# Performance work log

Hardware: AMD Instinct MI355X
Metric: run time of the kernel (lower is better)

## Reference

```python
import jax, jax.numpy as jnp
import numpy as np

N = 100000
DIN = 896        # 128 * 7, hard-coded as input_dim1 in hccexplorer_graph
HID = 256        # hidden_channels
HEADS = 1        # num_heads
L = 2            # num_layers
ALPHA = 0.5
EPS = 1e-5


def layernorm(x, g, b):
    m = jnp.mean(x, axis=-1, keepdims=True)
    v = jnp.mean((x - m) ** 2, axis=-1, keepdims=True)
    return (x - m) / jnp.sqrt(v + EPS) * g + b


def full_attention_conv(qs, ks, vs):
    # qs, ks, vs: [N, H, D]. NOTE: global Frobenius-norm normalization (no dim arg in torch.norm).
    n = qs.shape[0]
    qs = qs / jnp.linalg.norm(qs)
    ks = ks / jnp.linalg.norm(ks)
    kvs = jnp.einsum('lhm,lhd->hmd', ks, vs)                 # [H, D, D]
    attn_num = jnp.einsum('nhm,hmd->nhd', qs, kvs) + n * vs  # [N, H, D]
    ks_sum = jnp.sum(ks, axis=0)                             # [H, D]
    denom = jnp.einsum('nhm,hm->nh', qs, ks_sum)[..., None] + n
    return attn_num / denom                                  # [N, H, D]


def setup_inputs() -> dict:
    key = jax.random.key(0)
    ks = jax.random.split(key, 12)
    s_in = 1.0 / np.sqrt(DIN)
    s_h = 1.0 / np.sqrt(HID)
    inp = {
        'x': jax.random.normal(ks[0], (N, DIN), jnp.float32),
        'edge_index': jax.random.randint(ks[1], (2, 1600000), 0, N, jnp.int64),
        'fc_w': jax.random.uniform(ks[2], (DIN, HID), jnp.float32, -s_in, s_in),
        'fc_b': jax.random.uniform(ks[3], (HID,), jnp.float32, -s_in, s_in),
        'Wq': jax.random.uniform(ks[4], (L, HID, HEADS * HID), jnp.float32, -s_h, s_h),
        'Wk': jax.random.uniform(ks[5], (L, HID, HEADS * HID), jnp.float32, -s_h, s_h),
        'Wv': jax.random.uniform(ks[6], (L, HID, HEADS * HID), jnp.float32, -s_h, s_h),
        'bq': jax.random.uniform(ks[7], (L, HEADS * HID), jnp.float32, -s_h, s_h),
        'bk': jax.random.uniform(ks[8], (L, HEADS * HID), jnp.float32, -s_h, s_h),
        'bv': jax.random.uniform(ks[9], (L, HEADS * HID), jnp.float32, -s_h, s_h),
        'ln_g': 1.0 + 0.01 * jax.random.normal(ks[10], (L + 1, HID), jnp.float32),
        'ln_b': 0.01 * jax.random.normal(ks[11], (L + 1, HID), jnp.float32),
    }
    return inp


def reference(x, edge_index, fc_w, fc_b, Wq, Wk, Wv, bq, bk, bv, ln_g, ln_b):
    # TransConv.forward in eval mode (dropout disabled); edge_index unused by linear attention.
    h = x @ fc_w + fc_b
    h = layernorm(h, ln_g[0], ln_b[0])
    h = jax.nn.relu(h)
    prev = h
    for i in range(L):
        q = (h @ Wq[i] + bq[i]).reshape(-1, HEADS, HID)
        k = (h @ Wk[i] + bk[i]).reshape(-1, HEADS, HID)
        v = (h @ Wv[i] + bv[i]).reshape(-1, HEADS, HID)
        a = full_attention_conv(q, k, v).mean(axis=1)        # [N, HID]
        h = ALPHA * a + (1.0 - ALPHA) * prev                  # residual
        h = layernorm(h, ln_g[i + 1], ln_b[i + 1])
        prev = h
    return h
```

## Files before the change

### kernel.cpp

```cpp
#include <hip/hip_runtime.h>
#include <hip/hip_bf16.h>

#define GLOBAL_AS __attribute__((address_space(1)))
#define SHARED_AS __attribute__((address_space(3)))

typedef __attribute__((ext_vector_type(8))) __bf16 bf16x8;
typedef __attribute__((ext_vector_type(4))) float floatx4;

__device__ __forceinline__ void async_ld16(const void* g, void* l) {
    __builtin_amdgcn_global_load_lds((GLOBAL_AS void*)g, (SHARED_AS void*)l, 16, 0, 0);
}

__device__ __forceinline__ bf16x8 cvt8(float4 a, float4 b) {
    bf16x8 w;
    w[0] = (__bf16)a.x; w[1] = (__bf16)a.y; w[2] = (__bf16)a.z; w[3] = (__bf16)a.w;
    w[4] = (__bf16)b.x; w[5] = (__bf16)b.y; w[6] = (__bf16)b.z; w[7] = (__bf16)b.w;
    return w;
}

__global__ void __launch_bounds__(256) prep_kernel(
    const float* __restrict__ fc_w, const float* __restrict__ Wv,
    __bf16* __restrict__ fcwT, __bf16* __restrict__ WvT)
{
    int idx = blockIdx.x * 256 + threadIdx.x;
    if (idx < 256 * 896) {
        int n = idx / 896, k = idx - n * 896;
        fcwT[idx] = (__bf16)fc_w[k * 256 + n];
    } else {
        int j = idx - 256 * 896;
        int l = j >> 16;
        int r = j & 65535;
        int n = r >> 8, k = r & 255;
        WvT[j] = (__bf16)Wv[l * 65536 + k * 256 + n];
    }
}

template<int MODE>
__device__ __forceinline__ void ln_epilogue(
    floatx4 (&acc)[4][4], floatx4 (&hprev)[4][4],
    const float* __restrict__ bias, const float* __restrict__ g,
    const float* __restrict__ bb, __bf16* sH, void* scratch,
    float* __restrict__ Out, int m0, int M, int tid)
{
    const int wave = tid >> 6, lane = tid & 63;
    const int q = lane >> 4, c15 = lane & 15;
    const int wn = wave;

    float bj[4];
#pragma unroll
    for (int j = 0; j < 4; ++j) bj[j] = bias[wn * 64 + j * 16 + c15];
#pragma unroll
    for (int i = 0; i < 4; ++i)
#pragma unroll
        for (int j = 0; j < 4; ++j)
#pragma unroll
            for (int r = 0; r < 4; ++r) {
                float v = acc[i][j][r] + bj[j];
                if (MODE != 0) v = 0.5f * v + 0.5f * hprev[i][j][r];
                acc[i][j][r] = v;
            }

    float s[4][4], s2[4][4];
#pragma unroll
    for (int i = 0; i < 4; ++i)
#pragma unroll
        for (int r = 0; r < 4; ++r) {
            float t = 0.f, t2 = 0.f;
#pragma unroll
            for (int j = 0; j < 4; ++j) { float v = acc[i][j][r]; t += v; t2 += v * v; }
            s[i][r] = t; s2[i][r] = t2;
        }
#pragma unroll
    for (int m = 1; m < 16; m <<= 1)
#pragma unroll
        for (int i = 0; i < 4; ++i)
#pragma unroll
            for (int r = 0; r < 4; ++r) {
                s[i][r]  += __shfl_xor(s[i][r],  m);
                s2[i][r] += __shfl_xor(s2[i][r], m);
            }

    float2* part  = (float2*)scratch;
    float2* muinv = part + 256;
    if (c15 == 0) {
#pragma unroll
        for (int i = 0; i < 4; ++i)
#pragma unroll
            for (int r = 0; r < 4; ++r) {
                int rl = i * 16 + q * 4 + r;
                part[rl * 4 + wn] = make_float2(s[i][r], s2[i][r]);
            }
    }
    __syncthreads();
    if (tid < 64) {
        float S = 0.f, SS = 0.f;
#pragma unroll
        for (int w = 0; w < 4; ++w) { float2 p = part[tid * 4 + w]; S += p.x; SS += p.y; }
        float mu  = S * (1.f / 256.f);
        float var = SS * (1.f / 256.f) - mu * mu;
        muinv[tid] = make_float2(mu, rsqrtf(var + 1e-5f));
    }
    __syncthreads();

    float gj[4], bj2[4];
#pragma unroll
    for (int j = 0; j < 4; ++j) {
        int col = wn * 64 + j * 16 + c15;
        gj[j] = g[col]; bj2[j] = bb[col];
    }
#pragma unroll
    for (int i = 0; i < 4; ++i)
#pragma unroll
        for (int r = 0; r < 4; ++r) {
            int rl = i * 16 + q * 4 + r;
            float2 mi = muinv[rl];
#pragma unroll
            for (int j = 0; j < 4; ++j) {
                float y = (acc[i][j][r] - mi.x) * mi.y * gj[j] + bj2[j];
                if (MODE == 0) y = fmaxf(y, 0.f);
                int col = wn * 64 + j * 16 + c15;
                if (MODE < 2) {
                    hprev[i][j][r] = y;
                    int byte = rl * 512 + (((col >> 3) ^ (rl & 7)) << 4) + ((col & 7) << 1);
                    *(__bf16*)((char*)sH + byte) = (__bf16)y;
                } else {
                    int row = m0 + rl;
                    if (row < M) Out[(size_t)row * 256 + col] = y;
                }
            }
        }
}

__global__ void __launch_bounds__(256, 2) fused_net(
    const float* __restrict__ x, const __bf16* __restrict__ fcwT,
    const __bf16* __restrict__ WvT, const float* __restrict__ fc_b,
    const float* __restrict__ bv, const float* __restrict__ ln_g,
    const float* __restrict__ ln_b, float* __restrict__ Out, int M)
{
    __shared__ __align__(16) __bf16 sA[2][64 * 32];
    __shared__ __align__(16) __bf16 sB[2][256 * 32];
    __shared__ __align__(16) __bf16 sH[64 * 256];

    const int tid  = threadIdx.x;
    const int wave = tid >> 6, lane = tid & 63;
    const int m0   = blockIdx.x * 64;
    const int lrow = lane & 15;
    const int srow = tid >> 2;
    const int scol = (tid & 3) * 8;
    int aRow = m0 + srow; if (aRow > M - 1) aRow = M - 1;

    const int sw     = (tid & 3) ^ ((srow >> 1) & 3);
    const int sslot8 = sw * 8;
    const int aWoff  = srow * 64 + (sw << 4);
    const int fslotB = (((lane >> 4) ^ ((lrow >> 1) & 3)) << 4);
    const int hx     = lrow & 7;

    floatx4 acc[4][4], hprev[4][4];
#pragma unroll
    for (int i = 0; i < 4; ++i)
#pragma unroll
        for (int j = 0; j < 4; ++j) acc[i][j] = {0.f, 0.f, 0.f, 0.f};

    {
        const int K = 896, NIT = 28;
        float4 pf0, pf1;
        {
            const float* src = x + (size_t)aRow * K + scol;
            pf0 = *(const float4*)src; pf1 = *(const float4*)(src + 4);
            *(bf16x8*)((char*)sA[0] + aWoff) = cvt8(pf0, pf1);
        }
#pragma unroll
        for (int c = 0; c < 4; ++c)
            async_ld16(fcwT + (size_t)(c * 64 + srow) * K + sslot8,
                       (char*)sB[0] + c * 4096 + wave * 1024);

        for (int it = 0; it < NIT; ++it) {
            const int cur = it & 1, nxt = cur ^ 1;
            const int k1 = (it + 1) << 5;
            __syncthreads();
            const bool more = (it + 1 < NIT);
            if (more) {
                const float* src = x + (size_t)aRow * K + k1 + scol;
                pf0 = *(const float4*)src; pf1 = *(const float4*)(src + 4);
#pragma unroll
                for (int c = 0; c < 4; ++c)
                    async_ld16(fcwT + (size_t)(c * 64 + srow) * K + k1 + sslot8,
                               (char*)sB[nxt] + c * 4096 + wave * 1024);
            }
            bf16x8 aF[4], bF[4];
#pragma unroll
            for (int i = 0; i < 4; ++i)
                aF[i] = *(const bf16x8*)((char*)sA[cur] + (i * 16 + lrow) * 64 + fslotB);
#pragma unroll
            for (int j = 0; j < 4; ++j)
                bF[j] = *(const bf16x8*)((char*)sB[cur] + (wave * 64 + j * 16 + lrow) * 64 + fslotB);
#pragma unroll
            for (int i = 0; i < 4; ++i)
#pragma unroll
                for (int j = 0; j < 4; ++j)
                    acc[i][j] = __builtin_amdgcn_mfma_f32_16x16x32_bf16(aF[i], bF[j], acc[i][j], 0, 0, 0);
            if (more)
                *(bf16x8*)((char*)sA[nxt] + aWoff) = cvt8(pf0, pf1);
        }

#pragma unroll
        for (int c = 0; c < 4; ++c)
            async_ld16(WvT + (size_t)(c * 64 + srow) * 256 + sslot8,
                       (char*)sB[0] + c * 4096 + wave * 1024);

        ln_epilogue<0>(acc, hprev, fc_b, ln_g, ln_b, sH, (void*)sA, nullptr, m0, M, tid);
    }

    for (int l = 0; l < 2; ++l) {
        const __bf16* Bt = WvT + l * 65536;
#pragma unroll
        for (int i = 0; i < 4; ++i)
#pragma unroll
            for (int j = 0; j < 4; ++j) acc[i][j] = {0.f, 0.f, 0.f, 0.f};

        for (int it = 0; it < 8; ++it) {
            const int cur = it & 1, nxt = cur ^ 1;
            const int k1 = (it + 1) << 5;
            __syncthreads();
            if (it < 7) {
#pragma unroll
                for (int c = 0; c < 4; ++c)
                    async_ld16(Bt + (size_t)(c * 64 + srow) * 256 + k1 + sslot8,
                               (char*)sB[nxt] + c * 4096 + wave * 1024);
            }
            bf16x8 aF[4], bF[4];
            const int ks = (it << 2) + (lane >> 4);
#pragma unroll
            for (int i = 0; i < 4; ++i)
                aF[i] = *(const bf16x8*)((char*)sH + (i * 16 + lrow) * 512 + ((ks ^ hx) << 4));
#pragma unroll
            for (int j = 0; j < 4; ++j)
                bF[j] = *(const bf16x8*)((char*)sB[cur] + (wave * 64 + j * 16 + lrow) * 64 + fslotB);
#pragma unroll
            for (int i = 0; i < 4; ++i)
#pragma unroll
                for (int j = 0; j < 4; ++j)
                    acc[i][j] = __builtin_amdgcn_mfma_f32_16x16x32_bf16(aF[i], bF[j], acc[i][j], 0, 0, 0);
        }

        if (l == 0) {
#pragma unroll
            for (int c = 0; c < 4; ++c)
                async_ld16(WvT + 65536 + (size_t)(c * 64 + srow) * 256 + sslot8,
                           (char*)sB[0] + c * 4096 + wave * 1024);
            ln_epilogue<1>(acc, hprev, bv, ln_g + 256, ln_b + 256,
                           sH, (void*)sA, nullptr, m0, M, tid);
        } else {
            ln_epilogue<2>(acc, hprev, bv + 256, ln_g + 512, ln_b + 512,
                           sH, (void*)sA, Out, m0, M, tid);
        }
    }
}

extern "C" void kernel_launch(void* const* d_in, const int* in_sizes, int n_in,
                              void* d_out, int out_size, void* d_ws, size_t ws_size,
                              hipStream_t stream)
{
    const float* x    = (const float*)d_in[0];
    const float* fc_w = (const float*)d_in[2];
    const float* fc_b = (const float*)d_in[3];
    const float* Wv   = (const float*)d_in[6];
    const float* bv   = (const float*)d_in[9];
    const float* ln_g = (const float*)d_in[10];
    const float* ln_b = (const float*)d_in[11];

    const int M = in_sizes[0] / 896;

    char* ws = (char*)d_ws;
    __bf16* fcwT = (__bf16*)ws;
    __bf16* WvT  = (__bf16*)(ws + 458752);

    prep_kernel<<<1408, 256, 0, stream>>>(fc_w, Wv, fcwT, WvT);

    const int nblk = (M + 63) / 64;
    fused_net<<<nblk, 256, 0, stream>>>(x, fcwT, WvT, fc_b, bv, ln_g, ln_b,
                                        (float*)d_out, M);
}
```

Baseline: 788.4 us.

## Pre-swizzle weights into MFMA fragment layout and load B directly to registers

The prep kernel now writes fc_w and Wv in an order matching the MFMA B-fragment layout, so each lane loads its B fragments straight from global memory into registers with register double buffering. This removes the LDS staging buffer for B. The hprev residual registers are dropped and the previous activation is reread from the bf16 copy in LDS, which lowers register and LDS pressure so launch bounds can rise to 3 blocks per CU. The trade-off is that each wave now reads the weights from global memory or L2 separately instead of sharing one LDS copy, and the residual uses the bf16-rounded previous activation.

New measurement: 717.5 us. 1.1x faster.

```diff
diff --git a/kernel.cpp b/kernel.cpp
--- a/kernel.cpp
+++ b/kernel.cpp
@@ -1,15 +1,8 @@
 #include <hip/hip_runtime.h>
 #include <hip/hip_bf16.h>
 
-#define GLOBAL_AS __attribute__((address_space(1)))
-#define SHARED_AS __attribute__((address_space(3)))
-
 typedef __attribute__((ext_vector_type(8))) __bf16 bf16x8;
 typedef __attribute__((ext_vector_type(4))) float floatx4;
-
-__device__ __forceinline__ void async_ld16(const void* g, void* l) {
-    __builtin_amdgcn_global_load_lds((GLOBAL_AS void*)g, (SHARED_AS void*)l, 16, 0, 0);
-}
 
 __device__ __forceinline__ bf16x8 cvt8(float4 a, float4 b) {
     bf16x8 w;
@@ -23,42 +16,51 @@
     __bf16* __restrict__ fcwT, __bf16* __restrict__ WvT)
 {
     int idx = blockIdx.x * 256 + threadIdx.x;
-    if (idx < 256 * 896) {
-        int n = idx / 896, k = idx - n * 896;
+    if (idx < 229376) {
+        int k32 = idx >> 13, rem = idx & 8191;
+        int t = rem >> 9, q = (rem >> 7) & 3, c = (rem >> 3) & 15, e = rem & 7;
+        int n = t * 16 + c, k = k32 * 32 + q * 8 + e;
         fcwT[idx] = (__bf16)fc_w[k * 256 + n];
     } else {
-        int j = idx - 256 * 896;
-        int l = j >> 16;
-        int r = j & 65535;
-        int n = r >> 8, k = r & 255;
+        int j = idx - 229376;
+        int l = j >> 16, r = j & 65535;
+        int k32 = r >> 13, rem = r & 8191;
+        int t = rem >> 9, q = (rem >> 7) & 3, c = (rem >> 3) & 15, e = rem & 7;
+        int n = t * 16 + c, k = k32 * 32 + q * 8 + e;
         WvT[j] = (__bf16)Wv[l * 65536 + k * 256 + n];
     }
 }
 
 template<int MODE>
 __device__ __forceinline__ void ln_epilogue(
-    floatx4 (&acc)[4][4], floatx4 (&hprev)[4][4],
+    floatx4 (&acc)[4][4],
     const float* __restrict__ bias, const float* __restrict__ g,
-    const float* __restrict__ bb, __bf16* sH, void* scratch,
+    const float* __restrict__ bb, __bf16* sH, float2* sScr,
     float* __restrict__ Out, int m0, int M, int tid)
 {
     const int wave = tid >> 6, lane = tid & 63;
     const int q = lane >> 4, c15 = lane & 15;
-    const int wn = wave;
 
     float bj[4];
 #pragma unroll
-    for (int j = 0; j < 4; ++j) bj[j] = bias[wn * 64 + j * 16 + c15];
-#pragma unroll
-    for (int i = 0; i < 4; ++i)
-#pragma unroll
-        for (int j = 0; j < 4; ++j)
-#pragma unroll
-            for (int r = 0; r < 4; ++r) {
+    for (int j = 0; j < 4; ++j) bj[j] = bias[wave * 64 + j * 16 + c15];
+#pragma unroll
+    for (int i = 0; i < 4; ++i)
+#pragma unroll
+        for (int r = 0; r < 4; ++r) {
+            int rl = i * 16 + q * 4 + r;
+#pragma unroll
+            for (int j = 0; j < 4; ++j) {
                 float v = acc[i][j][r] + bj[j];
-                if (MODE != 0) v = 0.5f * v + 0.5f * hprev[i][j][r];
+                if (MODE != 0) {
+                    int col = wave * 64 + j * 16 + c15;
+                    int byte = rl * 512 + (((col >> 3) ^ (rl & 7)) << 4) + ((col & 7) << 1);
+                    float pv = (float)*(const __bf16*)((const char*)sH + byte);
+                    v = 0.5f * v + 0.5f * pv;
+                }
                 acc[i][j][r] = v;
             }
+        }
 
     float s[4][4], s2[4][4];
 #pragma unroll
@@ -80,15 +82,15 @@
                 s2[i][r] += __shfl_xor(s2[i][r], m);
             }
 
-    float2* part  = (float2*)scratch;
-    float2* muinv = part + 256;
+    float2* part  = sScr;
+    float2* muinv = sScr + 256;
     if (c15 == 0) {
 #pragma unroll
         for (int i = 0; i < 4; ++i)
 #pragma unroll
             for (int r = 0; r < 4; ++r) {
                 int rl = i * 16 + q * 4 + r;
-                part[rl * 4 + wn] = make_float2(s[i][r], s2[i][r]);
+                part[rl * 4 + wave] = make_float2(s[i][r], s2[i][r]);
             }
     }
     __syncthreads();
@@ -105,7 +107,7 @@
     float gj[4], bj2[4];
 #pragma unroll
     for (int j = 0; j < 4; ++j) {
-        int col = wn * 64 + j * 16 + c15;
+        int col = wave * 64 + j * 16 + c15;
         gj[j] = g[col]; bj2[j] = bb[col];
     }
 #pragma unroll
@@ -118,9 +120,8 @@
             for (int j = 0; j < 4; ++j) {
                 float y = (acc[i][j][r] - mi.x) * mi.y * gj[j] + bj2[j];
                 if (MODE == 0) y = fmaxf(y, 0.f);
-                int col = wn * 64 + j * 16 + c15;
+                int col = wave * 64 + j * 16 + c15;
                 if (MODE < 2) {
-                    hprev[i][j][r] = y;
                     int byte = rl * 512 + (((col >> 3) ^ (rl & 7)) << 4) + ((col & 7) << 1);
                     *(__bf16*)((char*)sH + byte) = (__bf16)y;
                 } else {
@@ -131,129 +132,117 @@
         }
 }
 
-__global__ void __launch_bounds__(256, 2) fused_net(
+__global__ void __launch_bounds__(256, 3) fused_net(
     const float* __restrict__ x, const __bf16* __restrict__ fcwT,
     const __bf16* __restrict__ WvT, const float* __restrict__ fc_b,
     const float* __restrict__ bv, const float* __restrict__ ln_g,
     const float* __restrict__ ln_b, float* __restrict__ Out, int M)
 {
     __shared__ __align__(16) __bf16 sA[2][64 * 32];
-    __shared__ __align__(16) __bf16 sB[2][256 * 32];
     __shared__ __align__(16) __bf16 sH[64 * 256];
+    __shared__ __align__(16) float2 sScr[320];
 
     const int tid  = threadIdx.x;
     const int wave = tid >> 6, lane = tid & 63;
     const int m0   = blockIdx.x * 64;
     const int lrow = lane & 15;
+    const int q4   = lane >> 4;
     const int srow = tid >> 2;
     const int scol = (tid & 3) * 8;
     int aRow = m0 + srow; if (aRow > M - 1) aRow = M - 1;
 
-    const int sw     = (tid & 3) ^ ((srow >> 1) & 3);
-    const int sslot8 = sw * 8;
-    const int aWoff  = srow * 64 + (sw << 4);
-    const int fslotB = (((lane >> 4) ^ ((lrow >> 1) & 3)) << 4);
-    const int hx     = lrow & 7;
-
-    floatx4 acc[4][4], hprev[4][4];
+    const int sw    = (tid & 3) ^ ((srow >> 1) & 3);
+    const int aWoff = srow * 64 + (sw << 4);
+    const int fslot = (q4 ^ ((lrow >> 1) & 3)) << 4;
+    const int hx    = lrow & 7;
+
+    floatx4 acc[4][4];
 #pragma unroll
     for (int i = 0; i < 4; ++i)
 #pragma unroll
         for (int j = 0; j < 4; ++j) acc[i][j] = {0.f, 0.f, 0.f, 0.f};
 
+    bf16x8 bF[4], bFn[4];
+
     {
-        const int K = 896, NIT = 28;
-        float4 pf0, pf1;
+        const int K = 896;
+        const __bf16* bPtr = fcwT + wave * 2048 + lane * 8;
+#pragma unroll
+        for (int j = 0; j < 4; ++j) bF[j] = *(const bf16x8*)(bPtr + j * 512);
         {
             const float* src = x + (size_t)aRow * K + scol;
-            pf0 = *(const float4*)src; pf1 = *(const float4*)(src + 4);
-            *(bf16x8*)((char*)sA[0] + aWoff) = cvt8(pf0, pf1);
-        }
-#pragma unroll
-        for (int c = 0; c < 4; ++c)
-            async_ld16(fcwT + (size_t)(c * 64 + srow) * K + sslot8,
-                       (char*)sB[0] + c * 4096 + wave * 1024);
-
-        for (int it = 0; it < NIT; ++it) {
+            float4 p0 = *(const float4*)src, p1 = *(const float4*)(src + 4);
+            *(bf16x8*)((char*)sA[0] + aWoff) = cvt8(p0, p1);
+        }
+
+        for (int it = 0; it < 28; ++it) {
             const int cur = it & 1, nxt = cur ^ 1;
-            const int k1 = (it + 1) << 5;
             __syncthreads();
-            const bool more = (it + 1 < NIT);
+            const bool more = (it + 1 < 28);
+            float4 p0, p1;
             if (more) {
-                const float* src = x + (size_t)aRow * K + k1 + scol;
-                pf0 = *(const float4*)src; pf1 = *(const float4*)(src + 4);
-#pragma unroll
-                for (int c = 0; c < 4; ++c)
-                    async_ld16(fcwT + (size_t)(c * 64 + srow) * K + k1 + sslot8,
-                               (char*)sB[nxt] + c * 4096 + wave * 1024);
-            }
-            bf16x8 aF[4], bF[4];
-#pragma unroll
-            for (int i = 0; i < 4; ++i)
-                aF[i] = *(const bf16x8*)((char*)sA[cur] + (i * 16 + lrow) * 64 + fslotB);
-#pragma unroll
-            for (int j = 0; j < 4; ++j)
-                bF[j] = *(const bf16x8*)((char*)sB[cur] + (wave * 64 + j * 16 + lrow) * 64 + fslotB);
+                const float* src = x + (size_t)aRow * K + ((it + 1) << 5) + scol;
+                p0 = *(const float4*)src; p1 = *(const float4*)(src + 4);
+#pragma unroll
+                for (int j = 0; j < 4; ++j)
+                    bFn[j] = *(const bf16x8*)(bPtr + (it + 1) * 8192 + j * 512);
+            }
+            bf16x8 aF[4];
+#pragma unroll
+            for (int i = 0; i < 4; ++i)
+                aF[i] = *(const bf16x8*)((char*)sA[cur] + (i * 16 + lrow) * 64 + fslot);
 #pragma unroll
             for (int i = 0; i < 4; ++i)
 #pragma unroll
                 for (int j = 0; j < 4; ++j)
                     acc[i][j] = __builtin_amdgcn_mfma_f32_16x16x32_bf16(aF[i], bF[j], acc[i][j], 0, 0, 0);
-            if (more)
-                *(bf16x8*)((char*)sA[nxt] + aWoff) = cvt8(pf0, pf1);
-        }
-
-#pragma unroll
-        for (int c = 0; c < 4; ++c)
-            async_ld16(WvT + (size_t)(c * 64 + srow) * 256 + sslot8,
-                       (char*)sB[0] + c * 4096 + wave * 1024);
-
-        ln_epilogue<0>(acc, hprev, fc_b, ln_g, ln_b, sH, (void*)sA, nullptr, m0, M, tid);
-    }
-
+            if (more) {
+                *(bf16x8*)((char*)sA[nxt] + aWoff) = cvt8(p0, p1);
+#pragma unroll
+                for (int j = 0; j < 4; ++j) bF[j] = bFn[j];
+            }
+        }
+        ln_epilogue<0>(acc, fc_b, ln_g, ln_b, sH, sScr, nullptr, m0, M, tid);
+    }
+
+#pragma unroll
     for (int l = 0; l < 2; ++l) {
-        const __bf16* Bt = WvT + l * 65536;
+        const __bf16* bPtr = WvT + l * 65536 + wave * 2048 + lane * 8;
 #pragma unroll
         for (int i = 0; i < 4; ++i)
 #pragma unroll
             for (int j = 0; j < 4; ++j) acc[i][j] = {0.f, 0.f, 0.f, 0.f};
+#pragma unroll
+        for (int j = 0; j < 4; ++j) bF[j] = *(const bf16x8*)(bPtr + j * 512);
+
+        __syncthreads();
 
         for (int it = 0; it < 8; ++it) {
-            const int cur = it & 1, nxt = cur ^ 1;
-            const int k1 = (it + 1) << 5;
-            __syncthreads();
             if (it < 7) {
 #pragma unroll
-                for (int c = 0; c < 4; ++c)
-                    async_ld16(Bt + (size_t)(c * 64 + srow) * 256 + k1 + sslot8,
-                               (char*)sB[nxt] + c * 4096 + wave * 1024);
-            }
-            bf16x8 aF[4], bF[4];
-            const int ks = (it << 2) + (lane >> 4);
+                for (int j = 0; j < 4; ++j)
+                    bFn[j] = *(const bf16x8*)(bPtr + (it + 1) * 8192 + j * 512);
+            }
+            bf16x8 aF[4];
+            const int ks = (it << 2) + q4;
 #pragma unroll
             for (int i = 0; i < 4; ++i)
                 aF[i] = *(const bf16x8*)((char*)sH + (i * 16 + lrow) * 512 + ((ks ^ hx) << 4));
 #pragma unroll
-            for (int j = 0; j < 4; ++j)
-                bF[j] = *(const bf16x8*)((char*)sB[cur] + (wave * 64 + j * 16 + lrow) * 64 + fslotB);
-#pragma unroll
             for (int i = 0; i < 4; ++i)
 #pragma unroll
                 for (int j = 0; j < 4; ++j)
                     acc[i][j] = __builtin_amdgcn_mfma_f32_16x16x32_bf16(aF[i], bF[j], acc[i][j], 0, 0, 0);
-        }
-
-        if (l == 0) {
-#pragma unroll
-            for (int c = 0; c < 4; ++c)
-                async_ld16(WvT + 65536 + (size_t)(c * 64 + srow) * 256 + sslot8,
-                           (char*)sB[0] + c * 4096 + wave * 1024);
-            ln_epilogue<1>(acc, hprev, bv, ln_g + 256, ln_b + 256,
-                           sH, (void*)sA, nullptr, m0, M, tid);
-        } else {
-            ln_epilogue<2>(acc, hprev, bv + 256, ln_g + 512, ln_b + 512,
-                           sH, (void*)sA, Out, m0, M, tid);
-        }
+            if (it < 7) {
+#pragma unroll
+                for (int j = 0; j < 4; ++j) bF[j] = bFn[j];
+            }
+        }
+
+        if (l == 0)
+            ln_epilogue<1>(acc, bv, ln_g + 256, ln_b + 256, sH, sScr, nullptr, m0, M, tid);
+        else
+            ln_epilogue<2>(acc, bv + 256, ln_g + 512, ln_b + 512, sH, sScr, Out, m0, M, tid);
     }
 }
 
```
